# Optimization experiments

Measured on AMD Instinct MI355X. Metric: run time of the kernel, lower is better.

Reference implementation:

```python
import jax, jax.numpy as jnp
import numpy as np

T = 2048
HIDDEN = 4096
H = 32
HKV = 8
D = 128
THETA = 10000.0


def setup_inputs() -> dict:
    key = jax.random.key(0)
    k1, k2, k3, k4, k5 = jax.random.split(key, 5)
    s = 0.02
    return {
        "x": jax.random.normal(k1, (T, 2 * HIDDEN), dtype=jnp.float32),
        "positions": jnp.arange(T, dtype=jnp.int32),
        "Wq": jax.random.normal(k2, (H * D, 2 * HIDDEN), dtype=jnp.float32) * s,
        "Wk": jax.random.normal(k3, (HKV * D, 2 * HIDDEN), dtype=jnp.float32) * s,
        "Wv": jax.random.normal(k4, (HKV * D, 2 * HIDDEN), dtype=jnp.float32) * s,
        "Wo": jax.random.normal(k5, (HIDDEN, H * D), dtype=jnp.float32) * s,
    }


def _rope_cos_sin(positions):
    # NeoX-style: cos_sin_cache[pos] = [cos(freqs), sin(freqs)], freqs over head_dim/2
    inv_freq = 1.0 / (THETA ** (jnp.arange(0, D, 2, dtype=jnp.float32) / D))
    freqs = positions.astype(jnp.float32)[:, None] * inv_freq  # [T, D/2]
    return jnp.cos(freqs)[:, None, :], jnp.sin(freqs)[:, None, :]  # broadcast over heads


def _apply_rope(t, cos, sin):
    half = D // 2
    t1, t2 = t[..., :half], t[..., half:]
    return jnp.concatenate([t1 * cos - t2 * sin, t2 * cos + t1 * sin], axis=-1)


def reference(x, positions, Wq, Wk, Wv, Wo):
    n = x.shape[0]
    q = (x @ Wq.T).reshape(n, H, D)
    k = (x @ Wk.T).reshape(n, HKV, D)
    v = (x @ Wv.T).reshape(n, HKV, D)
    cos, sin = _rope_cos_sin(positions)
    q = _apply_rope(q, cos, sin)
    k = _apply_rope(k, cos, sin)
    # cache starts empty -> k_full/v_full are just k/v; prefill (n>1) -> causal
    G = H // HKV  # GQA group size; avoid materializing repeated K/V
    qg = q.reshape(n, HKV, G, D)
    scale = D ** -0.5
    scores = jnp.einsum("tkgd,skd->kgts", qg, k) * scale  # [HKV, G, T, T]
    causal = jnp.arange(n)[:, None] >= jnp.arange(n)[None, :]
    scores = jnp.where(causal, scores, jnp.finfo(scores.dtype).min)
    p = jax.nn.softmax(scores, axis=-1)
    o = jnp.einsum("kgts,skd->tkgd", p, v).reshape(n, H * D)
    return o @ Wo.T
```

## Files before the change

### kernel.cpp

```cpp
#include <hip/hip_runtime.h>
#include <hip/hip_bf16.h>
#include <math.h>

typedef unsigned short u16;
typedef u16 u16x8 __attribute__((ext_vector_type(8)));
typedef __bf16 bf16x8 __attribute__((ext_vector_type(8)));
typedef float f32x4 __attribute__((ext_vector_type(4)));

#define T_SEQ 2048
#define IN_DIM 8192
#define QKV_COLS 6144
#define O_COLS 4096

__device__ __forceinline__ u16 f2bf(float f){
  unsigned u = __builtin_bit_cast(unsigned, f);
  u += 0x7fffu + ((u >> 16) & 1u);
  return (u16)(u >> 16);
}
__device__ __forceinline__ float bf2f(u16 h){
  unsigned u = ((unsigned)h) << 16;
  return __builtin_bit_cast(float, u);
}
__device__ __forceinline__ void gload16(const void* g, void* l){
  __builtin_amdgcn_global_load_lds((const __attribute__((address_space(1))) unsigned*)g,
                                   (__attribute__((address_space(3))) unsigned*)l, 16, 0, 0);
}
__device__ __forceinline__ void storeC(float* p, float v){ *p = v; }
__device__ __forceinline__ void storeC(u16* p, float v){ *p = f2bf(v); }

__global__ void cvt_f32_bf16(const float* __restrict__ s, u16* __restrict__ d, int n4){
  int stride = gridDim.x * blockDim.x;
  for (int i = blockIdx.x*blockDim.x + threadIdx.x; i < n4; i += stride){
    float4 v = ((const float4*)s)[i];
    ushort4 o;
    o.x = f2bf(v.x); o.y = f2bf(v.y); o.z = f2bf(v.z); o.w = f2bf(v.w);
    ((ushort4*)d)[i] = o;
  }
}

__global__ void rope_scale_kernel(u16* __restrict__ qkv, const int* __restrict__ pos){
  __shared__ float cs[64], sn[64];
  int t = blockIdx.x;
  int p = pos[t];
  if (threadIdx.x < 64){
    int i = threadIdx.x;
    double e = (double)(2*i) / 128.0;
    float invf = (float)pow(10000.0, -e);
    float ang = (float)p * invf;
    cs[i] = cosf(ang);
    sn[i] = sinf(ang);
  }
  __syncthreads();
  u16* row = qkv + (size_t)t * QKV_COLS;
  const float qscale = 0.08838834764831845f;
  for (int idx = threadIdx.x; idx < 40*64; idx += blockDim.x){
    int head = idx >> 6, i = idx & 63;
    int base = (head < 32) ? head*128 : 4096 + (head-32)*128;
    float sc = (head < 32) ? qscale : 1.0f;
    float t1 = bf2f(row[base + i]);
    float t2 = bf2f(row[base + i + 64]);
    row[base + i]      = f2bf((t1*cs[i] - t2*sn[i]) * sc);
    row[base + i + 64] = f2bf((t2*cs[i] + t1*sn[i]) * sc);
  }
}

template<typename OutT>
__global__ __launch_bounds__(256) void gemm_bt(const u16* __restrict__ A, const u16* __restrict__ B,
                                               OutT* __restrict__ C, int M, int N, int K, int ldc){
  __shared__ __attribute__((aligned(16))) u16 Asm[128*32];
  __shared__ __attribute__((aligned(16))) u16 Bsm[128*32];
  const int tid = threadIdx.x;
  const int l = tid & 63, w = tid >> 6;
  const int wm = w >> 1, wn = w & 1;
  const int lr = l & 15, lg = l >> 4;
  const int m0 = blockIdx.y * 128, n0 = blockIdx.x * 128;

  f32x4 acc[4][4] = {};

  const u16* Ag = A + (size_t)(m0 + (tid >> 2)) * K + (tid & 3) * 8;
  const u16* Bg = B + (size_t)(n0 + (tid >> 2)) * K + (tid & 3) * 8;
  u16* As0 = Asm + (w * 64) * 8;
  u16* Bs0 = Bsm + (w * 64) * 8;

  const int kiters = K >> 5;
  for (int kt = 0; kt < kiters; ++kt){
    const int kb = kt * 32;
    gload16(Ag + kb, As0);
    gload16(Ag + (size_t)64 * K + kb, As0 + 256*8);
    gload16(Bg + kb, Bs0);
    gload16(Bg + (size_t)64 * K + kb, Bs0 + 256*8);
    __syncthreads();
    bf16x8 af[4], bfr[4];
    #pragma unroll
    for (int mm = 0; mm < 4; ++mm)
      af[mm] = *(const bf16x8*)(Asm + (wm*64 + mm*16 + lr)*32 + lg*8);
    #pragma unroll
    for (int nn = 0; nn < 4; ++nn)
      bfr[nn] = *(const bf16x8*)(Bsm + (wn*64 + nn*16 + lr)*32 + lg*8);
    #pragma unroll
    for (int mm = 0; mm < 4; ++mm)
      #pragma unroll
      for (int nn = 0; nn < 4; ++nn)
        acc[mm][nn] = __builtin_amdgcn_mfma_f32_16x16x32_bf16(af[mm], bfr[nn], acc[mm][nn], 0, 0, 0);
    __syncthreads();
  }
  #pragma unroll
  for (int mm = 0; mm < 4; ++mm)
    #pragma unroll
    for (int nn = 0; nn < 4; ++nn)
      #pragma unroll
      for (int r = 0; r < 4; ++r){
        int row = m0 + wm*64 + mm*16 + lg*4 + r;
        int col = n0 + wn*64 + nn*16 + lr;
        storeC(&C[(size_t)row*ldc + col], acc[mm][nn][r]);
      }
}

__global__ __launch_bounds__(256) void attn_kernel(const u16* __restrict__ qkv, u16* __restrict__ ob){
  __shared__ __attribute__((aligned(16))) u16 Ksm[32*128];
  __shared__ __attribute__((aligned(16))) u16 Vt[128*40];
  __shared__ __attribute__((aligned(16))) u16 Psm[4][32*40];
  const int tid = threadIdx.x, l = tid & 63, w = tid >> 6;
  const int lr = l & 15, lg = l >> 4;
  const int qb = (gridDim.x - 1) - blockIdx.x;
  const int kv = blockIdx.y;
  const int h = kv*4 + w;
  const int q0 = qb * 32;

  bf16x8 aq[2][4];
  #pragma unroll
  for (int mm = 0; mm < 2; ++mm)
    #pragma unroll
    for (int kk = 0; kk < 4; ++kk)
      aq[mm][kk] = *(const bf16x8*)(qkv + (size_t)(q0 + mm*16 + lr)*QKV_COLS + h*128 + kk*32 + lg*8);

  f32x4 oacc[2][8] = {};
  float mrun[2][4], lrun[2][4];
  #pragma unroll
  for (int mm=0;mm<2;mm++)
    #pragma unroll
    for (int r=0;r<4;r++){ mrun[mm][r] = -1e30f; lrun[mm][r] = 0.f; }

  const int cbv = ((tid & 15) << 4) | (tid >> 4);
  for (int kt = 0; kt <= qb; ++kt){
    const int s0 = kt * 32;
    #pragma unroll
    for (int i = 0; i < 2; ++i){
      int c = tid + i*256, s = c >> 4, dq = c & 15;
      u16x8 kvv = *(const u16x8*)(qkv + (size_t)(s0+s)*QKV_COLS + 4096 + kv*128 + dq*8);
      int lin = (s << 8) + (dq << 4); lin ^= (s & 7) << 4;
      *(u16x8*)((char*)Ksm + lin) = kvv;
    }
    #pragma unroll
    for (int i = 0; i < 2; ++i){
      int c = cbv + i*256, s = c >> 4, dq = c & 15;
      u16x8 vv = *(const u16x8*)(qkv + (size_t)(s0+s)*QKV_COLS + 5120 + kv*128 + dq*8);
      #pragma unroll
      for (int j = 0; j < 8; ++j) Vt[(dq*8+j)*40 + s] = vv[j];
    }
    __syncthreads();

    f32x4 sa[2][2] = {};
    #pragma unroll
    for (int kk = 0; kk < 4; ++kk){
      bf16x8 bk[2];
      #pragma unroll
      for (int nn = 0; nn < 2; ++nn){
        int srow = nn*16 + lr;
        int lin = (srow << 8) + (kk << 6) + (lg << 4); lin ^= (srow & 7) << 4;
        bk[nn] = *(const bf16x8*)((char*)Ksm + lin);
      }
      #pragma unroll
      for (int mm = 0; mm < 2; ++mm)
        #pragma unroll
        for (int nn = 0; nn < 2; ++nn)
          sa[mm][nn] = __builtin_amdgcn_mfma_f32_16x16x32_bf16(aq[mm][kk], bk[nn], sa[mm][nn], 0,0,0);
    }

    if (kt == qb){
      #pragma unroll
      for (int mm=0;mm<2;mm++)
        #pragma unroll
        for (int nn=0;nn<2;nn++)
          #pragma unroll
          for (int r=0;r<4;r++){
            int qrel = mm*16 + lg*4 + r, srel = nn*16 + lr;
            if (srel > qrel) sa[mm][nn][r] = -1e30f;
          }
    }

    float alph[2][4];
    #pragma unroll
    for (int mm=0;mm<2;mm++)
      #pragma unroll
      for (int r=0;r<4;r++){
        float v = fmaxf(sa[mm][0][r], sa[mm][1][r]);
        v = fmaxf(v, __shfl_xor(v, 1));
        v = fmaxf(v, __shfl_xor(v, 2));
        v = fmaxf(v, __shfl_xor(v, 4));
        v = fmaxf(v, __shfl_xor(v, 8));
        float mn = fmaxf(mrun[mm][r], v);
        float al = __expf(mrun[mm][r] - mn);
        float p0 = __expf(sa[mm][0][r] - mn);
        float p1 = __expf(sa[mm][1][r] - mn);
        sa[mm][0][r] = p0; sa[mm][1][r] = p1;
        float rs = p0 + p1;
        rs += __shfl_xor(rs, 1);
        rs += __shfl_xor(rs, 2);
        rs += __shfl_xor(rs, 4);
        rs += __shfl_xor(rs, 8);
        lrun[mm][r] = lrun[mm][r]*al + rs;
        mrun[mm][r] = mn;
        alph[mm][r] = al;
      }
    #pragma unroll
    for (int mm=0;mm<2;mm++)
      #pragma unroll
      for (int df=0;df<8;df++)
        #pragma unroll
        for (int r=0;r<4;r++)
          oacc[mm][df][r] *= alph[mm][r];

    #pragma unroll
    for (int mm=0;mm<2;mm++)
      #pragma unroll
      for (int nn=0;nn<2;nn++)
        #pragma unroll
        for (int r=0;r<4;r++)
          Psm[w][(mm*16 + lg*4 + r)*40 + nn*16 + lr] = f2bf(sa[mm][nn][r]);

    bf16x8 ap[2];
    #pragma unroll
    for (int mm=0;mm<2;mm++)
      ap[mm] = *(const bf16x8*)(&Psm[w][(mm*16 + lr)*40 + lg*8]);
    #pragma unroll
    for (int df=0;df<8;df++){
      bf16x8 bv = *(const bf16x8*)(&Vt[(df*16 + lr)*40 + lg*8]);
      #pragma unroll
      for (int mm=0;mm<2;mm++)
        oacc[mm][df] = __builtin_amdgcn_mfma_f32_16x16x32_bf16(ap[mm], bv, oacc[mm][df], 0,0,0);
    }
    __syncthreads();
  }

  #pragma unroll
  for (int mm=0;mm<2;mm++)
    #pragma unroll
    for (int df=0;df<8;df++)
      #pragma unroll
      for (int r=0;r<4;r++){
        float val = oacc[mm][df][r] / lrun[mm][r];
        int t = q0 + mm*16 + lg*4 + r;
        int col = h*128 + df*16 + lr;
        ob[(size_t)t*O_COLS + col] = f2bf(val);
      }
}

extern "C" void kernel_launch(void* const* d_in, const int* in_sizes, int n_in,
                              void* d_out, int out_size, void* d_ws, size_t ws_size,
                              hipStream_t stream){
  const float* x  = (const float*)d_in[0];
  const int*   pos= (const int*)d_in[1];
  const float* Wq = (const float*)d_in[2];
  const float* Wk = (const float*)d_in[3];
  const float* Wv = (const float*)d_in[4];
  const float* Wo = (const float*)d_in[5];
  float* out = (float*)d_out;

  char* ws = (char*)d_ws;
  u16* xb   = (u16*)(ws);
  u16* wb   = (u16*)(ws + 33554432);
  u16* wob  = (u16*)(ws + 134217728);
  u16* qkv  = (u16*)(ws + 167772160);
  u16* obuf = (u16*)(ws + 192937984);

  cvt_f32_bf16<<<2048, 256, 0, stream>>>(x,  xb, (T_SEQ*IN_DIM)/4);
  cvt_f32_bf16<<<2048, 256, 0, stream>>>(Wq, wb, (4096*IN_DIM)/4);
  cvt_f32_bf16<<<1024, 256, 0, stream>>>(Wk, wb + (size_t)4096*IN_DIM, (1024*IN_DIM)/4);
  cvt_f32_bf16<<<1024, 256, 0, stream>>>(Wv, wb + (size_t)5120*IN_DIM, (1024*IN_DIM)/4);
  cvt_f32_bf16<<<2048, 256, 0, stream>>>(Wo, wob, (4096*4096)/4);

  gemm_bt<u16><<<dim3(48,16), 256, 0, stream>>>(xb, wb, qkv, 2048, 6144, 8192, 6144);
  rope_scale_kernel<<<T_SEQ, 256, 0, stream>>>(qkv, pos);
  attn_kernel<<<dim3(64,8), 256, 0, stream>>>(qkv, obuf);
  gemm_bt<float><<<dim3(32,16), 256, 0, stream>>>(obuf, wob, out, 2048, 4096, 4096, 4096);
}
```

Measured before the change: 935.2 us.

## Replace GEMM with 256x256-tile multi-buffered pipelined kernel and fuse conversion launches

Both projection GEMMs now use a 512-thread kernel with 256x256 output tiles, a 4-slot LDS ring that prefetches two K-steps ahead, swizzled LDS offsets, split A loads with interleaved MFMA phases and s_setprio. This targets the per-iteration load-then-barrier stalls and low data reuse of the old 128x128 kernel. The five f32-to-bf16 conversion launches are merged into one kernel. The risks are fewer blocks for the QKV GEMM (192 tiles over the CU count), a larger register footprint, and manually tuned waitcnt and barrier ordering.

Result: no change. 919.1 us (-1.7%).

```diff
diff --git a/kernel.cpp b/kernel.cpp
--- a/kernel.cpp
+++ b/kernel.cpp
@@ -28,13 +28,29 @@
 __device__ __forceinline__ void storeC(float* p, float v){ *p = v; }
 __device__ __forceinline__ void storeC(u16* p, float v){ *p = f2bf(v); }
 
-__global__ void cvt_f32_bf16(const float* __restrict__ s, u16* __restrict__ d, int n4){
+__global__ void cvt_all(const float* __restrict__ x, const float* __restrict__ wq,
+                        const float* __restrict__ wk, const float* __restrict__ wv,
+                        const float* __restrict__ wo,
+                        u16* __restrict__ xb, u16* __restrict__ wb, u16* __restrict__ wob){
+  const int NX  = T_SEQ*IN_DIM/4;
+  const int NQ  = 4096*IN_DIM/4;
+  const int NKV = 1024*IN_DIM/4;
+  const int NO  = 4096*4096/4;
+  const int TOT = NX + NQ + 2*NKV + NO;
   int stride = gridDim.x * blockDim.x;
-  for (int i = blockIdx.x*blockDim.x + threadIdx.x; i < n4; i += stride){
-    float4 v = ((const float4*)s)[i];
-    ushort4 o;
-    o.x = f2bf(v.x); o.y = f2bf(v.y); o.z = f2bf(v.z); o.w = f2bf(v.w);
-    ((ushort4*)d)[i] = o;
+  for (int i = blockIdx.x*blockDim.x + threadIdx.x; i < TOT; i += stride){
+    const float4* s; ushort4* d; int j = i;
+    if (j < NX){ s = (const float4*)x; d = (ushort4*)xb; }
+    else { j -= NX;
+      if (j < NQ){ s = (const float4*)wq; d = (ushort4*)wb; }
+      else { j -= NQ;
+        if (j < NKV){ s = (const float4*)wk; d = (ushort4*)(wb + (size_t)4096*IN_DIM); }
+        else { j -= NKV;
+          if (j < NKV){ s = (const float4*)wv; d = (ushort4*)(wb + (size_t)5120*IN_DIM); }
+          else { j -= NKV; s = (const float4*)wo; d = (ushort4*)wob; } } } }
+    float4 v = s[j];
+    ushort4 o; o.x = f2bf(v.x); o.y = f2bf(v.y); o.z = f2bf(v.z); o.w = f2bf(v.w);
+    d[j] = o;
   }
 }
 
@@ -65,54 +81,96 @@
 }
 
 template<typename OutT>
-__global__ __launch_bounds__(256) void gemm_bt(const u16* __restrict__ A, const u16* __restrict__ B,
-                                               OutT* __restrict__ C, int M, int N, int K, int ldc){
-  __shared__ __attribute__((aligned(16))) u16 Asm[128*32];
-  __shared__ __attribute__((aligned(16))) u16 Bsm[128*32];
+__global__ __launch_bounds__(512,2) void gemm_pipe(const u16* __restrict__ A, const u16* __restrict__ B,
+                                                   OutT* __restrict__ C, int K, int ldc){
+  __shared__ __attribute__((aligned(16))) u16 Asm[4*8192];
+  __shared__ __attribute__((aligned(16))) u16 Bsm[4*8192];
   const int tid = threadIdx.x;
-  const int l = tid & 63, w = tid >> 6;
-  const int wm = w >> 1, wn = w & 1;
+  const int w = tid >> 6, l = tid & 63;
+  const int wm = w >> 2, wn = w & 3;
   const int lr = l & 15, lg = l >> 4;
-  const int m0 = blockIdx.y * 128, n0 = blockIdx.x * 128;
-
-  f32x4 acc[4][4] = {};
-
-  const u16* Ag = A + (size_t)(m0 + (tid >> 2)) * K + (tid & 3) * 8;
-  const u16* Bg = B + (size_t)(n0 + (tid >> 2)) * K + (tid & 3) * 8;
-  u16* As0 = Asm + (w * 64) * 8;
-  u16* Bs0 = Bsm + (w * 64) * 8;
-
-  const int kiters = K >> 5;
-  for (int kt = 0; kt < kiters; ++kt){
-    const int kb = kt * 32;
-    gload16(Ag + kb, As0);
-    gload16(Ag + (size_t)64 * K + kb, As0 + 256*8);
-    gload16(Bg + kb, Bs0);
-    gload16(Bg + (size_t)64 * K + kb, Bs0 + 256*8);
-    __syncthreads();
-    bf16x8 af[4], bfr[4];
-    #pragma unroll
-    for (int mm = 0; mm < 4; ++mm)
-      af[mm] = *(const bf16x8*)(Asm + (wm*64 + mm*16 + lr)*32 + lg*8);
-    #pragma unroll
-    for (int nn = 0; nn < 4; ++nn)
-      bfr[nn] = *(const bf16x8*)(Bsm + (wn*64 + nn*16 + lr)*32 + lg*8);
-    #pragma unroll
-    for (int mm = 0; mm < 4; ++mm)
-      #pragma unroll
-      for (int nn = 0; nn < 4; ++nn)
-        acc[mm][nn] = __builtin_amdgcn_mfma_f32_16x16x32_bf16(af[mm], bfr[nn], acc[mm][nn], 0, 0, 0);
-    __syncthreads();
-  }
-  #pragma unroll
-  for (int mm = 0; mm < 4; ++mm)
-    #pragma unroll
-    for (int nn = 0; nn < 4; ++nn)
+  const int m0 = blockIdx.y * 256, n0 = blockIdx.x * 256;
+
+  const int srow  = tid >> 2;
+  const int sslot = ((tid & 3) - ((tid >> 3) & 3)) & 3;
+  const u16* Ag = A + (size_t)(m0 + srow) * K + sslot * 8;
+  const u16* Bg = B + (size_t)(n0 + srow) * K + sslot * 8;
+  char* AsB = (char*)Asm;
+  char* BsB = (char*)Bsm;
+  const int sdst = w * 1024;
+
+  int aoff[4], aoff2[4], boff[4];
+  #pragma unroll
+  for (int i = 0; i < 4; ++i){
+    int ra = wm*128 + i*16 + lr;
+    aoff[i]  = ra*64  + (((lg + (ra>>1)) & 3) << 4);
+    int ra2 = wm*128 + 64 + i*16 + lr;
+    aoff2[i] = ra2*64 + (((lg + (ra2>>1)) & 3) << 4);
+    int rb = wn*64 + i*16 + lr;
+    boff[i]  = rb*64  + (((lg + (rb>>1)) & 3) << 4);
+  }
+
+  f32x4 acc[8][4] = {};
+  const int NT = K >> 5;
+
+  #pragma unroll
+  for (int t = 0; t < 2; ++t){
+    gload16(Ag + t*32,                    AsB + t*16384 +        sdst);
+    gload16(Ag + (size_t)128*K + t*32,    AsB + t*16384 + 8192 + sdst);
+    gload16(Bg + t*32,                    BsB + t*16384 +        sdst);
+    gload16(Bg + (size_t)128*K + t*32,    BsB + t*16384 + 8192 + sdst);
+  }
+
+  for (int t = 0; t < NT; ++t){
+    const int bb = (t & 3) * 16384;
+    if (t == NT-1) asm volatile("s_waitcnt vmcnt(0)" ::: "memory");
+    else           asm volatile("s_waitcnt vmcnt(4)" ::: "memory");
+    __builtin_amdgcn_s_barrier();
+    bf16x8 bfr[4], afr[4];
+    #pragma unroll
+    for (int n = 0; n < 4; ++n) bfr[n] = *(const bf16x8*)(BsB + bb + boff[n]);
+    #pragma unroll
+    for (int i = 0; i < 4; ++i) afr[i] = *(const bf16x8*)(AsB + bb + aoff[i]);
+    if (t + 2 < NT){
+      const int nb = ((t+2) & 3) * 16384;
+      gload16(Ag + (t+2)*32,                 AsB + nb +        sdst);
+      gload16(Ag + (size_t)128*K + (t+2)*32, AsB + nb + 8192 + sdst);
+    }
+    __builtin_amdgcn_s_barrier();
+    __builtin_amdgcn_s_setprio(1);
+    #pragma unroll
+    for (int i = 0; i < 4; ++i)
+      #pragma unroll
+      for (int n = 0; n < 4; ++n)
+        acc[i][n] = __builtin_amdgcn_mfma_f32_16x16x32_bf16(afr[i], bfr[n], acc[i][n], 0, 0, 0);
+    __builtin_amdgcn_s_setprio(0);
+    bf16x8 afr2[4];
+    #pragma unroll
+    for (int i = 0; i < 4; ++i) afr2[i] = *(const bf16x8*)(AsB + bb + aoff2[i]);
+    if (t + 2 < NT){
+      const int nb = ((t+2) & 3) * 16384;
+      gload16(Bg + (t+2)*32,                 BsB + nb +        sdst);
+      gload16(Bg + (size_t)128*K + (t+2)*32, BsB + nb + 8192 + sdst);
+    }
+    __builtin_amdgcn_s_barrier();
+    __builtin_amdgcn_s_setprio(1);
+    #pragma unroll
+    for (int i = 0; i < 4; ++i)
+      #pragma unroll
+      for (int n = 0; n < 4; ++n)
+        acc[4+i][n] = __builtin_amdgcn_mfma_f32_16x16x32_bf16(afr2[i], bfr[n], acc[4+i][n], 0, 0, 0);
+    __builtin_amdgcn_s_setprio(0);
+  }
+
+  #pragma unroll
+  for (int m = 0; m < 8; ++m)
+    #pragma unroll
+    for (int n = 0; n < 4; ++n)
       #pragma unroll
       for (int r = 0; r < 4; ++r){
-        int row = m0 + wm*64 + mm*16 + lg*4 + r;
-        int col = n0 + wn*64 + nn*16 + lr;
-        storeC(&C[(size_t)row*ldc + col], acc[mm][nn][r]);
+        int row = m0 + wm*128 + m*16 + lg*4 + r;
+        int col = n0 + wn*64 + n*16 + lr;
+        storeC(&C[(size_t)row*ldc + col], acc[m][n][r]);
       }
 }
 
@@ -274,14 +332,10 @@
   u16* qkv  = (u16*)(ws + 167772160);
   u16* obuf = (u16*)(ws + 192937984);
 
-  cvt_f32_bf16<<<2048, 256, 0, stream>>>(x,  xb, (T_SEQ*IN_DIM)/4);
-  cvt_f32_bf16<<<2048, 256, 0, stream>>>(Wq, wb, (4096*IN_DIM)/4);
-  cvt_f32_bf16<<<1024, 256, 0, stream>>>(Wk, wb + (size_t)4096*IN_DIM, (1024*IN_DIM)/4);
-  cvt_f32_bf16<<<1024, 256, 0, stream>>>(Wv, wb + (size_t)5120*IN_DIM, (1024*IN_DIM)/4);
-  cvt_f32_bf16<<<2048, 256, 0, stream>>>(Wo, wob, (4096*4096)/4);
-
-  gemm_bt<u16><<<dim3(48,16), 256, 0, stream>>>(xb, wb, qkv, 2048, 6144, 8192, 6144);
+  cvt_all<<<2048, 256, 0, stream>>>(x, Wq, Wk, Wv, Wo, xb, wb, wob);
+
+  gemm_pipe<u16><<<dim3(24,8), 512, 0, stream>>>(xb, wb, qkv, IN_DIM, QKV_COLS);
   rope_scale_kernel<<<T_SEQ, 256, 0, stream>>>(qkv, pos);
   attn_kernel<<<dim3(64,8), 256, 0, stream>>>(qkv, obuf);
-  gemm_bt<float><<<dim3(32,16), 256, 0, stream>>>(obuf, wob, out, 2048, 4096, 4096, 4096);
-}
+  gemm_pipe<float><<<dim3(16,8), 512, 0, stream>>>(obuf, wob, out, O_COLS, O_COLS);
+}
```
